# Performance work log

Hardware: AMD Instinct MI355X
Metric: run time of the kernel (lower is better)

The kernel has to match this reference:

```python
import jax, jax.numpy as jnp
import numpy as np

K_ORDER, NUM_HEADS, BETA = 4, 2, 0.5
D_IN, D_OUT = 64, 64


def _batch_and_pos(n_nodes, N):
    # batch[i] = graph id of node i; pos[i] = index of node i within its graph
    batch = jnp.repeat(jnp.arange(n_nodes.shape[0], dtype=jnp.int32), n_nodes, total_repeat_length=N)
    ptr = jnp.concatenate([jnp.zeros(1, jnp.int32), jnp.cumsum(n_nodes).astype(jnp.int32)])
    pos = jnp.arange(N, dtype=jnp.int32) - ptr[batch]
    return batch, pos


def _to_pad(feat, batch, pos, Bsz, max_node):
    out_shape = (Bsz, max_node) + feat.shape[1:]
    return jnp.zeros(out_shape, feat.dtype).at[batch, pos].set(feat)


def fast_attn_conv(qs, ks, vs, n_nodes, batch, pos, max_node):
    # qs/ks/vs: [N,H,D]; linear attention with per-graph kv outer-product sums
    Bsz = n_nodes.shape[0]
    q_pad = _to_pad(qs, batch, pos, Bsz, max_node)  # [B,M,H,D]
    k_pad = _to_pad(ks, batch, pos, Bsz, max_node)
    v_pad = _to_pad(vs, batch, pos, Bsz, max_node)
    kv = jnp.einsum('bnhd,bnhe->bdhe', k_pad, v_pad)  # [B,D,H,D]
    v_sum = jax.ops.segment_sum(vs, batch, num_segments=Bsz)  # [B,H,D]
    k_sum = jax.ops.segment_sum(ks, batch, num_segments=Bsz)  # [B,H,D]
    numerator = jnp.einsum('bnhd,bdhe->bnhe', q_pad, kv)[batch, pos] + v_sum[batch]
    denom = jnp.einsum('bnhd,bhd->bnh', q_pad, k_sum)[batch, pos]
    denom = denom + n_nodes.astype(qs.dtype)[batch][:, None]
    return numerator / denom[..., None]


def gcn_conv(x, edge_index, e_feat):
    # x: [N,H,D], e_feat: [E,D]
    N = x.shape[0]
    row, col = edge_index[0], edge_index[1]
    deg = jax.ops.segment_sum(jnp.ones(row.shape[0], x.dtype), row, num_segments=N)
    dis = jnp.where(deg > 0, deg ** -0.5, jnp.zeros_like(deg))
    w = dis[row] * dis[col]  # [E]
    msg_edge = jax.ops.segment_sum(w[:, None] * e_feat, row, num_segments=N)  # [N,D]
    new_feat = jax.ops.segment_sum(x[col] * w[:, None, None], row, num_segments=N)  # [N,H,D]
    return new_feat + msg_edge[:, None, :]


def setup_inputs():
    key = jax.random.key(0)
    ks = jax.random.split(key, 10)
    B = 64
    n_nodes_np = np.tile(np.array([1000, 2000], np.int32), B // 2)  # sums to 96000
    N = int(n_nodes_np.sum())
    E = 768000
    x = jax.random.normal(ks[0], (N, D_IN), jnp.float32)
    edge_index = jax.random.randint(ks[1], (2, E), 0, N, jnp.int32)
    edge_attr = jax.random.randint(ks[2], (E, 3), 0, 8, jnp.int32)
    s = 0.02
    Wq_w = jax.random.normal(ks[3], (D_IN * NUM_HEADS, D_IN), jnp.float32) * s
    Wq_b = jnp.zeros((D_IN * NUM_HEADS,), jnp.float32)
    Wk_w = jax.random.normal(ks[4], (D_IN * NUM_HEADS, D_IN), jnp.float32) * s
    Wk_b = jnp.zeros((D_IN * NUM_HEADS,), jnp.float32)
    Wo_w = jax.random.normal(ks[5], (D_OUT, D_IN * NUM_HEADS), jnp.float32) * s
    Wo_b = jnp.zeros((D_OUT,), jnp.float32)
    bond_emb = jax.random.normal(ks[6], (3, 8, D_OUT), jnp.float32) * s
    return {"x": x, "Wq_w": Wq_w, "Wq_b": Wq_b, "Wk_w": Wk_w, "Wk_b": Wk_b,
            "Wo_w": Wo_w, "Wo_b": Wo_b, "bond_emb": bond_emb,
            "edge_index": edge_index, "edge_attr": edge_attr,
            "n_nodes": jnp.asarray(n_nodes_np)}


def reference(x, Wq_w, Wq_b, Wk_w, Wk_b, Wo_w, Wo_b, bond_emb, edge_index, edge_attr, n_nodes):
    N = x.shape[0]
    max_node = 2000  # static max over n_nodes
    batch, pos = _batch_and_pos(n_nodes, N)
    query = (x @ Wq_w.T + Wq_b).reshape(N, NUM_HEADS, D_IN)
    key_t = (x @ Wk_w.T + Wk_b).reshape(N, NUM_HEADS, D_IN)
    qs = query / jnp.linalg.norm(query, axis=2, keepdims=True)
    kk = key_t / jnp.linalg.norm(key_t, axis=2, keepdims=True)
    # BondEncoder: sum of per-feature embeddings
    e_feat = bond_emb[0][edge_attr[:, 0]] + bond_emb[1][edge_attr[:, 1]] + bond_emb[2][edge_attr[:, 2]]
    h = jnp.broadcast_to(x[:, None, :], (N, NUM_HEADS, D_IN))
    acc = h
    cur = h
    for _ in range(K_ORDER):
        gcn_i = gcn_conv(cur, edge_index, e_feat)
        attn_i = fast_attn_conv(qs, kk, cur, n_nodes, batch, pos, max_node)
        cur = BETA * gcn_i + (1.0 - BETA) * attn_i
        acc = acc + cur
    out = acc.reshape(N, NUM_HEADS * D_IN)
    return (out @ Wo_w.T + Wo_b) / NUM_HEADS
```

## Files before the change

kernel.cpp:

```cpp
#include <hip/hip_runtime.h>
#include <hip/hip_bf16.h>


typedef __attribute__((ext_vector_type(8))) short bf16x8;
typedef __attribute__((ext_vector_type(4))) float f32x4v;

#define CHUNK 100

__device__ __forceinline__ float asf(unsigned int u) { union { unsigned int i; float f; } v; v.i = u; return v.f; }
__device__ __forceinline__ float b2f_u(unsigned short u) { return asf((unsigned int)u << 16); }
__device__ __forceinline__ unsigned short f2b_u(float f) {
    __hip_bfloat16 h = __float2bfloat16(f);
    union { __hip_bfloat16 h; unsigned short u; } v; v.h = h; return v.u;
}
__device__ __forceinline__ unsigned int pack2(float a, float b) {
    return (unsigned int)f2b_u(a) | ((unsigned int)f2b_u(b) << 16);
}
__device__ __forceinline__ float wave_reduce_sum(float v) {
    #pragma unroll
    for (int off = 32; off > 0; off >>= 1) v += __shfl_xor(v, off, 64);
    return v;
}

__global__ void k_ptr(const int* __restrict__ nn, int* __restrict__ ptr,
                      int* __restrict__ cptr, int* __restrict__ tptr, int B) {
    if (threadIdx.x == 0 && blockIdx.x == 0) {
        int s = 0, c = 0, t = 0; ptr[0] = 0; cptr[0] = 0; tptr[0] = 0;
        for (int i = 0; i < B; ++i) {
            s += nn[i]; ptr[i + 1] = s;
            c += (nn[i] + CHUNK - 1) / CHUNK; cptr[i + 1] = c;
            t += (nn[i] + 15) / 16; tptr[i + 1] = t;
        }
    }
}

__global__ void k_batch(const int* __restrict__ ptr, int* __restrict__ batch) {
    int b = blockIdx.x;
    int s = ptr[b], e = ptr[b + 1];
    for (int i = s + threadIdx.x; i < e; i += blockDim.x) batch[i] = b;
}

__global__ void k_wcvt(const float* __restrict__ Wq_w, const float* __restrict__ Wk_w,
                       const float* __restrict__ Wo_w, unsigned short* __restrict__ Wb) {
    int i = blockIdx.x * 256 + threadIdx.x;
    if (i < 24576) {
        float v = (i < 8192) ? Wq_w[i] : ((i < 16384) ? Wk_w[i - 8192] : Wo_w[i - 16384]);
        Wb[i] = f2b_u(v);
    }
}

__global__ __launch_bounds__(256) void k_qkm(
    const float* __restrict__ x, const unsigned short* __restrict__ Wb,
    const float* __restrict__ Wq_b, const float* __restrict__ Wk_b,
    unsigned short* __restrict__ q, unsigned short* __restrict__ kq,
    unsigned short* __restrict__ curA, int N)
{
    int w = threadIdx.x >> 6, l = threadIdx.x & 63;
    int six = l & 15, quad = l >> 4;
    int base = (blockIdx.x * 4 + w) * 16;
    if (base >= N) return;
    int n = base + six;
    int nc = min(n, N - 1);

    const float* xr = x + (size_t)nc * 64;
    float xv0[8], xv1[8];
    #pragma unroll
    for (int j = 0; j < 8; ++j) { xv0[j] = xr[quad * 8 + j]; xv1[j] = xr[32 + quad * 8 + j]; }
    union { bf16x8 v; unsigned int u[4]; } b0, b1;
    #pragma unroll
    for (int i = 0; i < 4; ++i) {
        b0.u[i] = pack2(xv0[2 * i], xv0[2 * i + 1]);
        b1.u[i] = pack2(xv1[2 * i], xv1[2 * i + 1]);
    }
    if (n < N) {
        unsigned short* cr = curA + (size_t)n * 128;
        *(uint4*)(cr + quad * 8)       = make_uint4(b0.u[0], b0.u[1], b0.u[2], b0.u[3]);
        *(uint4*)(cr + 32 + quad * 8)  = make_uint4(b1.u[0], b1.u[1], b1.u[2], b1.u[3]);
        *(uint4*)(cr + 64 + quad * 8)  = make_uint4(b0.u[0], b0.u[1], b0.u[2], b0.u[3]);
        *(uint4*)(cr + 96 + quad * 8)  = make_uint4(b1.u[0], b1.u[1], b1.u[2], b1.u[3]);
    }

    #pragma unroll
    for (int g = 0; g < 4; ++g) {
        f32x4v c[4];
        #pragma unroll
        for (int tt = 0; tt < 4; ++tt) {
            int t = g * 4 + tt;
            const unsigned short* wr = Wb + (size_t)(t * 16 + six) * 64;
            bf16x8 a0 = *(const bf16x8*)(wr + quad * 8);
            bf16x8 a1 = *(const bf16x8*)(wr + 32 + quad * 8);
            f32x4v cc = {0.f, 0.f, 0.f, 0.f};
            cc = __builtin_amdgcn_mfma_f32_16x16x32_bf16(a0, b0.v, cc, 0, 0, 0);
            cc = __builtin_amdgcn_mfma_f32_16x16x32_bf16(a1, b1.v, cc, 0, 0, 0);
            c[tt] = cc;
        }
        const float* bias = (g < 2) ? Wq_b : Wk_b;
        int cb = (g & 1) * 64 + quad * 4;
        float ss = 0.f;
        #pragma unroll
        for (int tt = 0; tt < 4; ++tt)
            #pragma unroll
            for (int r = 0; r < 4; ++r) {
                float v = c[tt][r] + bias[cb + tt * 16 + r];
                c[tt][r] = v;
                ss += v * v;
            }
        ss += __shfl_xor(ss, 16, 64);
        ss += __shfl_xor(ss, 32, 64);
        float sc = rsqrtf(ss);
        if (n < N) {
            unsigned short* dst = ((g < 2) ? q : kq) + (size_t)n * 128;
            #pragma unroll
            for (int tt = 0; tt < 4; ++tt) {
                unsigned int u0 = pack2(c[tt][0] * sc, c[tt][1] * sc);
                unsigned int u1 = pack2(c[tt][2] * sc, c[tt][3] * sc);
                *(uint2*)(dst + cb + tt * 16) = make_uint2(u0, u1);
            }
        }
    }
}

__global__ void k_deg(const int* __restrict__ row, int* __restrict__ deg,
                      int* __restrict__ slot, int E) {
    int e = blockIdx.x * 256 + threadIdx.x;
    if (e < E) slot[e] = atomicAdd(&deg[row[e]], 1);
}

__global__ void k_dis(const int* __restrict__ deg, float* __restrict__ dis, int N) {
    int n = blockIdx.x * 256 + threadIdx.x;
    if (n < N) { int d = deg[n]; dis[n] = d > 0 ? rsqrtf((float)d) : 0.f; }
}

__global__ void k_scan1(const int* __restrict__ deg, int* __restrict__ rowstart,
                        int* __restrict__ bsum, int N) {
    __shared__ int sh[256];
    int t = threadIdx.x, n = blockIdx.x * 256 + t;
    int v = (n < N) ? deg[n] : 0;
    sh[t] = v; __syncthreads();
    #pragma unroll
    for (int off = 1; off < 256; off <<= 1) {
        int add = (t >= off) ? sh[t - off] : 0;
        __syncthreads();
        sh[t] += add;
        __syncthreads();
    }
    if (n < N) rowstart[n] = sh[t] - v;
    if (t == 255) bsum[blockIdx.x] = sh[255];
}

__global__ void k_scan2(int* __restrict__ bsum, int nb) {
    __shared__ int sh[512];
    __shared__ int carry;
    int t = threadIdx.x;
    if (t == 0) carry = 0;
    __syncthreads();
    for (int base = 0; base < nb; base += 512) {
        int idx = base + t;
        int v = (idx < nb) ? bsum[idx] : 0;
        sh[t] = v; __syncthreads();
        for (int off = 1; off < 512; off <<= 1) {
            int add = (t >= off) ? sh[t - off] : 0;
            __syncthreads();
            sh[t] += add;
            __syncthreads();
        }
        if (idx < nb) bsum[idx] = sh[t] - v + carry;
        __syncthreads();
        if (t == 0) carry += sh[511];
        __syncthreads();
    }
}

__global__ void k_scan3(int* __restrict__ rowstart, const int* __restrict__ bsum, int N, int E) {
    int n = blockIdx.x * 256 + threadIdx.x;
    if (n < N) rowstart[n] += bsum[blockIdx.x];
    if (n == 0) rowstart[N] = E;
}

__global__ void k_fill(const int* __restrict__ eidx, const float* __restrict__ dis,
                       const int* __restrict__ rowstart, const int* __restrict__ slot,
                       int4* __restrict__ csr_pack, const int* __restrict__ eattr, int E) {
    int e = blockIdx.x * 256 + threadIdx.x;
    if (e >= E) return;
    int r = eidx[e], c = eidx[E + e];
    float wv = dis[r] * dis[c];
    int a0 = eattr[e * 3 + 0], a1 = eattr[e * 3 + 1], a2 = eattr[e * 3 + 2];
    int idx = rowstart[r] + slot[e];
    int4 v;
    v.x = c;
    v.y = __float_as_int(wv);
    v.z = a0 | (a1 << 8) | (a2 << 16);
    v.w = 0;
    csr_pack[idx] = v;
}

__global__ __launch_bounds__(256) void k_msg(
    const int* __restrict__ rowstart, const int4* __restrict__ csr_pack,
    const float* __restrict__ bond, unsigned short* __restrict__ msgb, int N) {
    __shared__ float bl[1536];
    int t = threadIdx.x, w = t >> 6, l = t & 63;
    for (int i = t; i < 1536; i += 256) bl[i] = bond[i];
    __syncthreads();
    for (int n = blockIdx.x * 4 + w; n < N; n += gridDim.x * 4) {
        int s0 = rowstart[n], s1 = rowstart[n + 1];
        float m = 0.f;
        #pragma unroll 4
        for (int i = s0; i < s1; ++i) {
            int4 pk = csr_pack[i];
            float wv = __int_as_float(pk.y);
            int att = pk.z;
            m += wv * (bl[(att & 255) * 64 + l] + bl[(8 + ((att >> 8) & 255)) * 64 + l]
                     + bl[(16 + (att >> 16)) * 64 + l]);
        }
        msgb[(size_t)n * 64 + l] = f2b_u(m);
    }
}

__global__ __launch_bounds__(256) void k_ksump(
    const unsigned short* __restrict__ kq, const int* __restrict__ ptr,
    const int* __restrict__ cptr, float* __restrict__ partKS, int B)
{
    int cid = blockIdx.x;
    if (cid >= cptr[B]) return;
    int lo = 0, hi = B - 1;
    while (lo < hi) { int mid = (lo + hi + 1) >> 1; if (cptr[mid] <= cid) lo = mid; else hi = mid - 1; }
    int b = lo;
    int start = ptr[b] + (cid - cptr[b]) * CHUNK;
    int end = min(start + CHUNK, ptr[b + 1]);
    int t = threadIdx.x, r = t >> 7, col = t & 127;
    float a = 0.f;
    for (int n = start + r; n < end; n += 2)
        a += b2f_u(kq[(size_t)n * 128 + col]);
    __shared__ float sh[256];
    sh[t] = a;
    __syncthreads();
    if (t < 128) partKS[(size_t)cid * 128 + t] = sh[t] + sh[t + 128];
}

__global__ __launch_bounds__(128) void k_ksr(
    const float* __restrict__ partKS, const int* __restrict__ cptr,
    float* __restrict__ ksum, int B)
{
    int b = blockIdx.x, t = threadIdx.x;
    float s = 0.f;
    int c0 = cptr[b], c1 = cptr[b + 1];
    for (int c = c0; c < c1; ++c) s += partKS[(size_t)c * 128 + t];
    ksum[b * 128 + t] = s;
}

__global__ __launch_bounds__(256) void k_denom(
    const unsigned short* __restrict__ q, const float* __restrict__ ksum,
    const int* __restrict__ batch, const int* __restrict__ nn,
    float* __restrict__ denom, int N)
{
    int w = threadIdx.x >> 6, l = threadIdx.x & 63;
    int n = blockIdx.x * 4 + w;
    if (n >= N) return;
    int b = batch[n];
    float d0 = b2f_u(q[(size_t)n * 128 + l]) * ksum[b * 128 + l];
    float d1 = b2f_u(q[(size_t)n * 128 + 64 + l]) * ksum[b * 128 + 64 + l];
    d0 = wave_reduce_sum(d0);
    d1 = wave_reduce_sum(d1);
    if (l == 0) {
        float nf = (float)nn[b];
        denom[n * 2 + 0] = d0 + nf;
        denom[n * 2 + 1] = d1 + nf;
    }
}

__global__ __launch_bounds__(256) void k_kvp(
    const unsigned short* __restrict__ kq, const unsigned short* __restrict__ cur,
    const int* __restrict__ ptr, const int* __restrict__ cptr,
    float* __restrict__ partKV, float* __restrict__ partVS, int B)
{
    int cid = blockIdx.x;
    if (cid >= cptr[B]) return;
    int lo = 0, hi = B - 1;
    while (lo < hi) { int mid = (lo + hi + 1) >> 1; if (cptr[mid] <= cid) lo = mid; else hi = mid - 1; }
    int b = lo;
    int start = ptr[b] + (cid - cptr[b]) * CHUNK;
    int end = min(start + CHUNK, ptr[b + 1]);

    int w = threadIdx.x >> 6, l = threadIdx.x & 63;
    int h = w >> 1, dhalf = w & 1;
    int d0 = dhalf * 32 + (l & 7) * 4;
    int e0 = (l >> 3) * 8;
    float a[4][8], va[8];
    #pragma unroll
    for (int i = 0; i < 4; ++i)
        #pragma unroll
        for (int j = 0; j < 8; ++j) a[i][j] = 0.f;
    #pragma unroll
    for (int j = 0; j < 8; ++j) va[j] = 0.f;

    const unsigned short* kp = kq + (size_t)start * 128 + h * 64 + d0;
    const unsigned short* vp = cur + (size_t)start * 128 + h * 64 + e0;
    #pragma unroll 4
    for (int n = start; n < end; ++n) {
        uint2 ku = *(const uint2*)kp;
        uint4 vu = *(const uint4*)vp;
        kp += 128; vp += 128;
        float k0 = asf(ku.x << 16), k1 = asf(ku.x & 0xffff0000u);
        float k2 = asf(ku.y << 16), k3 = asf(ku.y & 0xffff0000u);
        float v[8];
        v[0] = asf(vu.x << 16); v[1] = asf(vu.x & 0xffff0000u);
        v[2] = asf(vu.y << 16); v[3] = asf(vu.y & 0xffff0000u);
        v[4] = asf(vu.z << 16); v[5] = asf(vu.z & 0xffff0000u);
        v[6] = asf(vu.w << 16); v[7] = asf(vu.w & 0xffff0000u);
        #pragma unroll
        for (int j = 0; j < 8; ++j) {
            a[0][j] += k0 * v[j]; a[1][j] += k1 * v[j];
            a[2][j] += k2 * v[j]; a[3][j] += k3 * v[j];
            va[j] += v[j];
        }
    }
    float* dst = partKV + (size_t)cid * 8192 + h * 4096;
    #pragma unroll
    for (int j = 0; j < 8; ++j) {
        float4 s4 = { a[0][j], a[1][j], a[2][j], a[3][j] };
        *(float4*)(dst + (e0 + j) * 64 + d0) = s4;
    }
    if (dhalf == 0 && (l & 7) == 0) {
        float* vdst = partVS + (size_t)cid * 128 + h * 64 + e0;
        #pragma unroll
        for (int j = 0; j < 8; ++j) vdst[j] = va[j];
    }
}

__global__ __launch_bounds__(256) void k_red(
    const float* __restrict__ partKV, const float* __restrict__ partVS,
    const int* __restrict__ cptr, unsigned short* __restrict__ kvT_b,
    float* __restrict__ vsum, int B)
{
    int bid = blockIdx.x;
    int gh = bid >> 1, half = bid & 1;
    int g = gh >> 1, h = gh & 1;
    int c0 = cptr[g], c1 = cptr[g + 1];
    int t = threadIdx.x;
    int off = half * 2048 + t * 8;
    float s[8];
    #pragma unroll
    for (int i = 0; i < 8; ++i) s[i] = 0.f;
    for (int c = c0; c < c1; ++c) {
        const float4* src = (const float4*)(partKV + (size_t)c * 8192 + h * 4096 + off);
        #pragma unroll
        for (int i = 0; i < 2; ++i) {
            float4 v = src[i];
            s[i * 4 + 0] += v.x; s[i * 4 + 1] += v.y; s[i * 4 + 2] += v.z; s[i * 4 + 3] += v.w;
        }
    }
    unsigned int u[4];
    #pragma unroll
    for (int i = 0; i < 4; ++i) u[i] = pack2(s[2 * i], s[2 * i + 1]);
    *(uint4*)(kvT_b + (size_t)gh * 4096 + off) = make_uint4(u[0], u[1], u[2], u[3]);
    if (half == 0 && t < 64) {
        float vs = 0.f;
        for (int c = c0; c < c1; ++c) vs += partVS[(size_t)c * 128 + h * 64 + t];
        vsum[g * 128 + h * 64 + t] = vs;
    }
}

__global__ __launch_bounds__(256) void k_attn(
    const unsigned short* __restrict__ q, const unsigned short* __restrict__ kvT,
    const float* __restrict__ vsum, const float* __restrict__ denom,
    const int* __restrict__ ptr, const int* __restrict__ tptr,
    unsigned short* __restrict__ curB, int B)
{
    int w = threadIdx.x >> 6, l = threadIdx.x & 63;
    int tid = blockIdx.x * 4 + w;
    if (tid >= tptr[B]) return;
    int lo = 0, hi = B - 1;
    while (lo < hi) { int mid = (lo + hi + 1) >> 1; if (tptr[mid] <= tid) lo = mid; else hi = mid - 1; }
    int b0 = lo;
    int start = ptr[b0] + (tid - tptr[b0]) * 16;
    int end = min(start + 16, ptr[b0 + 1]);
    int quad = l >> 4, six = l & 15;
    int n = start + six;
    int nc = min(n, end - 1);
    bool live = n < end;
    #pragma unroll
    for (int h = 0; h < 2; ++h) {
        const unsigned short* qrow = q + (size_t)nc * 128 + h * 64;
        bf16x8 qb0 = *(const bf16x8*)(qrow + quad * 8);
        bf16x8 qb1 = *(const bf16x8*)(qrow + 32 + quad * 8);
        const unsigned short* Bb = kvT + (size_t)(b0 * 2 + h) * 4096;
        float dn = denom[nc * 2 + h];
        const float* vsb = vsum + (b0 * 2 + h) * 64;
        #pragma unroll
        for (int et = 0; et < 4; ++et) {
            const unsigned short* arow = Bb + (size_t)(et * 16 + six) * 64;
            bf16x8 a0 = *(const bf16x8*)(arow + quad * 8);
            bf16x8 a1 = *(const bf16x8*)(arow + 32 + quad * 8);
            f32x4v c = {0.f, 0.f, 0.f, 0.f};
            c = __builtin_amdgcn_mfma_f32_16x16x32_bf16(a0, qb0, c, 0, 0, 0);
            c = __builtin_amdgcn_mfma_f32_16x16x32_bf16(a1, qb1, c, 0, 0, 0);
            float4 vs = *(const float4*)(vsb + et * 16 + quad * 4);
            float v0 = 0.5f * (c[0] + vs.x) / dn;
            float v1 = 0.5f * (c[1] + vs.y) / dn;
            float v2 = 0.5f * (c[2] + vs.z) / dn;
            float v3 = 0.5f * (c[3] + vs.w) / dn;
            if (live) {
                uint2 st = make_uint2(pack2(v0, v1), pack2(v2, v3));
                *(uint2*)(curB + (size_t)n * 128 + h * 64 + et * 16 + quad * 4) = st;
            }
        }
    }
}

__global__ __launch_bounds__(256) void k_gcn(
    const unsigned short* __restrict__ curA, const unsigned short* __restrict__ msgb,
    const int* __restrict__ rowstart, const int4* __restrict__ csr_pack,
    unsigned short* __restrict__ curB, unsigned short* __restrict__ acc, int N, int first)
{
    int orig = blockIdx.x, nwg = gridDim.x;
    int q8 = nwg >> 3, r8 = nwg & 7;
    int xcd = orig & 7, j = orig >> 3;
    int swz = (xcd < r8 ? xcd * (q8 + 1) : r8 * (q8 + 1) + (xcd - r8) * q8) + j;

    int w = threadIdx.x >> 6, l = threadIdx.x & 63;
    int qq = l >> 4, ql = l & 15;
    int n = swz * 4 + w;
    if (n >= N) return;
    int s0 = rowstart[n], s1 = rowstart[n + 1];
    float g[8];
    #pragma unroll
    for (int j2 = 0; j2 < 8; ++j2) g[j2] = 0.f;
    #pragma unroll 2
    for (int i = s0 + qq; i < s1; i += 4) {
        int4 pk = csr_pack[i];
        float wv = __int_as_float(pk.y);
        uint4 u = *(const uint4*)(curA + (size_t)pk.x * 128 + 8 * ql);
        g[0] += wv * asf(u.x << 16); g[1] += wv * asf(u.x & 0xffff0000u);
        g[2] += wv * asf(u.y << 16); g[3] += wv * asf(u.y & 0xffff0000u);
        g[4] += wv * asf(u.z << 16); g[5] += wv * asf(u.z & 0xffff0000u);
        g[6] += wv * asf(u.w << 16); g[7] += wv * asf(u.w & 0xffff0000u);
    }
    #pragma unroll
    for (int j2 = 0; j2 < 8; ++j2) {
        g[j2] += __shfl_xor(g[j2], 16, 64);
        g[j2] += __shfl_xor(g[j2], 32, 64);
    }
    float g0 = (qq == 0) ? g[0] : (qq == 1) ? g[2] : (qq == 2) ? g[4] : g[6];
    float g1 = (qq == 0) ? g[1] : (qq == 1) ? g[3] : (qq == 2) ? g[5] : g[7];
    int e0 = 8 * ql + 2 * qq;
    unsigned int um = *(const unsigned int*)(msgb + (size_t)n * 64 + (e0 & 63));
    float mx = asf(um << 16), my = asf(um & 0xffff0000u);
    size_t o = (size_t)n * 128 + e0;
    unsigned int ub = *(const unsigned int*)(curB + o);
    float v0 = 0.5f * (g0 + mx) + asf(ub << 16);
    float v1 = 0.5f * (g1 + my) + asf(ub & 0xffff0000u);
    *(unsigned int*)(curB + o) = pack2(v0, v1);
    unsigned int ua = *(const unsigned int*)(first ? (curA + o) : (acc + o));
    *(unsigned int*)(acc + o) = pack2(asf(ua << 16) + v0, asf(ua & 0xffff0000u) + v1);
}

__global__ __launch_bounds__(256) void k_outm(
    const unsigned short* __restrict__ acc, const unsigned short* __restrict__ Wob,
    const float* __restrict__ Wo_b, float* __restrict__ out, int N)
{
    int w = threadIdx.x >> 6, l = threadIdx.x & 63;
    int six = l & 15, quad = l >> 4;
    int base = (blockIdx.x * 4 + w) * 16;
    if (base >= N) return;
    int n = base + six;
    int nc = min(n, N - 1);
    const unsigned short* ar = acc + (size_t)nc * 128;
    bf16x8 b0 = *(const bf16x8*)(ar + quad * 8);
    bf16x8 b1 = *(const bf16x8*)(ar + 32 + quad * 8);
    bf16x8 b2 = *(const bf16x8*)(ar + 64 + quad * 8);
    bf16x8 b3 = *(const bf16x8*)(ar + 96 + quad * 8);
    #pragma unroll
    for (int t = 0; t < 4; ++t) {
        const unsigned short* wr = Wob + (size_t)(t * 16 + six) * 128;
        bf16x8 a0 = *(const bf16x8*)(wr + quad * 8);
        bf16x8 a1 = *(const bf16x8*)(wr + 32 + quad * 8);
        bf16x8 a2 = *(const bf16x8*)(wr + 64 + quad * 8);
        bf16x8 a3 = *(const bf16x8*)(wr + 96 + quad * 8);
        f32x4v c = {0.f, 0.f, 0.f, 0.f};
        c = __builtin_amdgcn_mfma_f32_16x16x32_bf16(a0, b0, c, 0, 0, 0);
        c = __builtin_amdgcn_mfma_f32_16x16x32_bf16(a1, b1, c, 0, 0, 0);
        c = __builtin_amdgcn_mfma_f32_16x16x32_bf16(a2, b2, c, 0, 0, 0);
        c = __builtin_amdgcn_mfma_f32_16x16x32_bf16(a3, b3, c, 0, 0, 0);
        if (n < N) {
            float4 bias = *(const float4*)(Wo_b + t * 16 + quad * 4);
            float4 o4;
            o4.x = (c[0] + bias.x) * 0.5f;
            o4.y = (c[1] + bias.y) * 0.5f;
            o4.z = (c[2] + bias.z) * 0.5f;
            o4.w = (c[3] + bias.w) * 0.5f;
            *(float4*)(out + (size_t)n * 64 + t * 16 + quad * 4) = o4;
        }
    }
}

extern "C" void kernel_launch(void* const* d_in, const int* in_sizes, int n_in,
                              void* d_out, int out_size, void* d_ws, size_t ws_size,
                              hipStream_t stream) {
    const float* x    = (const float*)d_in[0];
    const float* Wq_w = (const float*)d_in[1];
    const float* Wq_b = (const float*)d_in[2];
    const float* Wk_w = (const float*)d_in[3];
    const float* Wk_b = (const float*)d_in[4];
    const float* Wo_w = (const float*)d_in[5];
    const float* Wo_b = (const float*)d_in[6];
    const float* bond = (const float*)d_in[7];
    const int*   eidx = (const int*)d_in[8];
    const int*   eattr= (const int*)d_in[9];
    const int*   nn   = (const int*)d_in[10];
    float* out = (float*)d_out;
    int N = in_sizes[0] / 64;
    int E = in_sizes[9] / 3;
    int B = in_sizes[10];

    char* p = (char*)d_ws;
    auto alloc = [&](size_t bytes) { char* r = p; p += (bytes + 255) & ~(size_t)255; return r; };
    unsigned short* q    = (unsigned short*)alloc((size_t)N * 128 * 2);
    unsigned short* kq   = (unsigned short*)alloc((size_t)N * 128 * 2);
    unsigned short* curA = (unsigned short*)alloc((size_t)N * 128 * 2);
    unsigned short* curB = (unsigned short*)alloc((size_t)N * 128 * 2);
    unsigned short* acc  = (unsigned short*)alloc((size_t)N * 128 * 2);
    int maxchunks = (N + CHUNK - 1) / CHUNK + B;
    int maxtiles  = (N + 15) / 16 + B;
    float* partKV = (float*)alloc((size_t)maxchunks * 8192 * 4);
    float* partVS = (float*)alloc((size_t)maxchunks * 128 * 4);
    float* partKS = (float*)alloc((size_t)maxchunks * 128 * 4);
    unsigned short* kvT_b = (unsigned short*)alloc((size_t)B * 2 * 64 * 64 * 2);
    float* vsum  = (float*)alloc((size_t)B * 128 * 4);
    float* ksum  = (float*)alloc((size_t)B * 128 * 4);
    float* denom = (float*)alloc((size_t)N * 2 * 4);
    float* dis   = (float*)alloc((size_t)N * 4);
    int* deg     = (int*)alloc((size_t)N * 4);
    int* rowstart= (int*)alloc((size_t)(N + 1) * 4);
    int* slot    = (int*)alloc((size_t)E * 4);
    int4* csr_pack = (int4*)alloc((size_t)E * 16);
    int* batch   = (int*)alloc((size_t)N * 4);
    int* ptr     = (int*)alloc((size_t)(B + 1) * 4);
    int* cptr    = (int*)alloc((size_t)(B + 1) * 4);
    int* tptr    = (int*)alloc((size_t)(B + 1) * 4);
    unsigned short* Wb = (unsigned short*)alloc(24576 * 2);
    int nb = (N + 255) / 256;
    int* bsum    = (int*)alloc((size_t)nb * 4);
    unsigned short* msgb = (unsigned short*)out;

    hipMemsetAsync(deg, 0, (size_t)N * 4, stream);

    k_ptr  <<<1, 64, 0, stream>>>(nn, ptr, cptr, tptr, B);
    k_batch<<<B, 256, 0, stream>>>(ptr, batch);
    k_wcvt <<<96, 256, 0, stream>>>(Wq_w, Wk_w, Wo_w, Wb);
    k_qkm  <<<(N + 63) / 64, 256, 0, stream>>>(x, Wb, Wq_b, Wk_b, q, kq, curA, N);
    k_deg  <<<(E + 255) / 256, 256, 0, stream>>>(eidx, deg, slot, E);
    k_dis  <<<(N + 255) / 256, 256, 0, stream>>>(deg, dis, N);
    k_scan1<<<nb, 256, 0, stream>>>(deg, rowstart, bsum, N);
    k_scan2<<<1, 512, 0, stream>>>(bsum, nb);
    k_scan3<<<nb, 256, 0, stream>>>(rowstart, bsum, N, E);
    k_fill <<<(E + 255) / 256, 256, 0, stream>>>(eidx, dis, rowstart, slot, csr_pack, eattr, E);
    k_msg  <<<2048, 256, 0, stream>>>(rowstart, csr_pack, bond, msgb, N);
    k_ksump<<<maxchunks, 256, 0, stream>>>(kq, ptr, cptr, partKS, B);
    k_ksr  <<<B, 128, 0, stream>>>(partKS, cptr, ksum, B);
    k_denom<<<(N + 3) / 4, 256, 0, stream>>>(q, ksum, batch, nn, denom, N);

    for (int it = 0; it < 4; ++it) {
        k_kvp <<<maxchunks, 256, 0, stream>>>(kq, curA, ptr, cptr, partKV, partVS, B);
        k_red <<<B * 4, 256, 0, stream>>>(partKV, partVS, cptr, kvT_b, vsum, B);
        k_attn<<<(maxtiles + 3) / 4, 256, 0, stream>>>(q, kvT_b, vsum, denom, ptr, tptr, curB, B);
        k_gcn <<<(N + 3) / 4, 256, 0, stream>>>(curA, msgb, rowstart, csr_pack, curB, acc, N, it == 0 ? 1 : 0);
        unsigned short* tmp = curA; curA = curB; curB = tmp;
    }
    k_outm<<<(N + 63) / 64, 256, 0, stream>>>(acc, Wb + 16384, Wo_b, out, N);
}
```

Before: 792.9 us.

## Process two GCN rows per wave and fold edge message into attention kernel

The GCN kernel now has each wave handle two consecutive CSR rows over their combined edge range. It keeps a total accumulator and one for row A, and recovers row B by subtraction, which balances work across short rows and halves the wave count. The per-node bond-message add moves into the attention epilogue, and the GCN kernel reads only weight and column from the packed CSR entry. Recovering row B by subtraction can add floating-point cancellation error, and the loop now does twice the FMAs per edge.

```diff
diff --git a/kernel.cpp b/kernel.cpp
--- a/kernel.cpp
+++ b/kernel.cpp
@@ -364,6 +364,7 @@
     const unsigned short* __restrict__ q, const unsigned short* __restrict__ kvT,
     const float* __restrict__ vsum, const float* __restrict__ denom,
     const int* __restrict__ ptr, const int* __restrict__ tptr,
+    const unsigned short* __restrict__ msgb,
     unsigned short* __restrict__ curB, int B)
 {
     int w = threadIdx.x >> 6, l = threadIdx.x & 63;
@@ -378,6 +379,10 @@
     int n = start + six;
     int nc = min(n, end - 1);
     bool live = n < end;
+    const unsigned short* mrow = msgb + (size_t)nc * 64;
+    uint2 me[4];
+    #pragma unroll
+    for (int et = 0; et < 4; ++et) me[et] = *(const uint2*)(mrow + et * 16 + quad * 4);
     #pragma unroll
     for (int h = 0; h < 2; ++h) {
         const unsigned short* qrow = q + (size_t)nc * 128 + h * 64;
@@ -395,10 +400,12 @@
             c = __builtin_amdgcn_mfma_f32_16x16x32_bf16(a0, qb0, c, 0, 0, 0);
             c = __builtin_amdgcn_mfma_f32_16x16x32_bf16(a1, qb1, c, 0, 0, 0);
             float4 vs = *(const float4*)(vsb + et * 16 + quad * 4);
-            float v0 = 0.5f * (c[0] + vs.x) / dn;
-            float v1 = 0.5f * (c[1] + vs.y) / dn;
-            float v2 = 0.5f * (c[2] + vs.z) / dn;
-            float v3 = 0.5f * (c[3] + vs.w) / dn;
+            float m0 = asf(me[et].x << 16), m1 = asf(me[et].x & 0xffff0000u);
+            float m2 = asf(me[et].y << 16), m3 = asf(me[et].y & 0xffff0000u);
+            float v0 = 0.5f * (c[0] + vs.x) / dn + 0.5f * m0;
+            float v1 = 0.5f * (c[1] + vs.y) / dn + 0.5f * m1;
+            float v2 = 0.5f * (c[2] + vs.z) / dn + 0.5f * m2;
+            float v3 = 0.5f * (c[3] + vs.w) / dn + 0.5f * m3;
             if (live) {
                 uint2 st = make_uint2(pack2(v0, v1), pack2(v2, v3));
                 *(uint2*)(curB + (size_t)n * 128 + h * 64 + et * 16 + quad * 4) = st;
@@ -408,50 +415,81 @@
 }
 
 __global__ __launch_bounds__(256) void k_gcn(
-    const unsigned short* __restrict__ curA, const unsigned short* __restrict__ msgb,
+    const unsigned short* __restrict__ curA,
     const int* __restrict__ rowstart, const int4* __restrict__ csr_pack,
     unsigned short* __restrict__ curB, unsigned short* __restrict__ acc, int N, int first)
 {
     int orig = blockIdx.x, nwg = gridDim.x;
     int q8 = nwg >> 3, r8 = nwg & 7;
-    int xcd = orig & 7, j = orig >> 3;
-    int swz = (xcd < r8 ? xcd * (q8 + 1) : r8 * (q8 + 1) + (xcd - r8) * q8) + j;
+    int xcd = orig & 7, jj = orig >> 3;
+    int swz = (xcd < r8 ? xcd * (q8 + 1) : r8 * (q8 + 1) + (xcd - r8) * q8) + jj;
 
     int w = threadIdx.x >> 6, l = threadIdx.x & 63;
     int qq = l >> 4, ql = l & 15;
-    int n = swz * 4 + w;
-    if (n >= N) return;
-    int s0 = rowstart[n], s1 = rowstart[n + 1];
-    float g[8];
-    #pragma unroll
-    for (int j2 = 0; j2 < 8; ++j2) g[j2] = 0.f;
+    int nA = swz * 8 + w * 2;
+    if (nA >= N) return;
+    bool hasB = (nA + 1) < N;
+    int s0  = rowstart[nA];
+    int sA1 = rowstart[nA + 1];
+    int s1  = hasB ? rowstart[nA + 2] : sA1;
+
+    int e0 = 8 * ql + 2 * qq;
+    size_t oA = (size_t)nA * 128 + e0;
+    size_t oB = (size_t)(nA + 1) * 128 + e0;
+    const unsigned short* accsrc = first ? curA : acc;
+    unsigned int ubA = *(const unsigned int*)(curB + oA);
+    unsigned int uaA = *(const unsigned int*)(accsrc + oA);
+    unsigned int ubB = 0, uaB = 0;
+    if (hasB) {
+        ubB = *(const unsigned int*)(curB + oB);
+        uaB = *(const unsigned int*)(accsrc + oB);
+    }
+
+    float gT[8], gA[8];
+    #pragma unroll
+    for (int j = 0; j < 8; ++j) { gT[j] = 0.f; gA[j] = 0.f; }
+    const int2* cw2 = (const int2*)csr_pack;
     #pragma unroll 2
     for (int i = s0 + qq; i < s1; i += 4) {
-        int4 pk = csr_pack[i];
-        float wv = __int_as_float(pk.y);
-        uint4 u = *(const uint4*)(curA + (size_t)pk.x * 128 + 8 * ql);
-        g[0] += wv * asf(u.x << 16); g[1] += wv * asf(u.x & 0xffff0000u);
-        g[2] += wv * asf(u.y << 16); g[3] += wv * asf(u.y & 0xffff0000u);
-        g[4] += wv * asf(u.z << 16); g[5] += wv * asf(u.z & 0xffff0000u);
-        g[6] += wv * asf(u.w << 16); g[7] += wv * asf(u.w & 0xffff0000u);
-    }
-    #pragma unroll
-    for (int j2 = 0; j2 < 8; ++j2) {
-        g[j2] += __shfl_xor(g[j2], 16, 64);
-        g[j2] += __shfl_xor(g[j2], 32, 64);
-    }
-    float g0 = (qq == 0) ? g[0] : (qq == 1) ? g[2] : (qq == 2) ? g[4] : g[6];
-    float g1 = (qq == 0) ? g[1] : (qq == 1) ? g[3] : (qq == 2) ? g[5] : g[7];
-    int e0 = 8 * ql + 2 * qq;
-    unsigned int um = *(const unsigned int*)(msgb + (size_t)n * 64 + (e0 & 63));
-    float mx = asf(um << 16), my = asf(um & 0xffff0000u);
-    size_t o = (size_t)n * 128 + e0;
-    unsigned int ub = *(const unsigned int*)(curB + o);
-    float v0 = 0.5f * (g0 + mx) + asf(ub << 16);
-    float v1 = 0.5f * (g1 + my) + asf(ub & 0xffff0000u);
-    *(unsigned int*)(curB + o) = pack2(v0, v1);
-    unsigned int ua = *(const unsigned int*)(first ? (curA + o) : (acc + o));
-    *(unsigned int*)(acc + o) = pack2(asf(ua << 16) + v0, asf(ua & 0xffff0000u) + v1);
+        int2 cw = cw2[2 * i];
+        float wv = __int_as_float(cw.y);
+        float wvA = (i < sA1) ? wv : 0.f;
+        uint4 u = *(const uint4*)(curA + (size_t)cw.x * 128 + 8 * ql);
+        float v0 = asf(u.x << 16), v1 = asf(u.x & 0xffff0000u);
+        float v2 = asf(u.y << 16), v3 = asf(u.y & 0xffff0000u);
+        float v4 = asf(u.z << 16), v5 = asf(u.z & 0xffff0000u);
+        float v6 = asf(u.w << 16), v7 = asf(u.w & 0xffff0000u);
+        gT[0] += wv * v0;  gA[0] += wvA * v0;
+        gT[1] += wv * v1;  gA[1] += wvA * v1;
+        gT[2] += wv * v2;  gA[2] += wvA * v2;
+        gT[3] += wv * v3;  gA[3] += wvA * v3;
+        gT[4] += wv * v4;  gA[4] += wvA * v4;
+        gT[5] += wv * v5;  gA[5] += wvA * v5;
+        gT[6] += wv * v6;  gA[6] += wvA * v6;
+        gT[7] += wv * v7;  gA[7] += wvA * v7;
+    }
+    #pragma unroll
+    for (int j = 0; j < 8; ++j) {
+        gT[j] += __shfl_xor(gT[j], 16, 64);
+        gT[j] += __shfl_xor(gT[j], 32, 64);
+        gA[j] += __shfl_xor(gA[j], 16, 64);
+        gA[j] += __shfl_xor(gA[j], 32, 64);
+    }
+    float a0 = (qq == 0) ? gA[0] : (qq == 1) ? gA[2] : (qq == 2) ? gA[4] : gA[6];
+    float a1 = (qq == 0) ? gA[1] : (qq == 1) ? gA[3] : (qq == 2) ? gA[5] : gA[7];
+    float t0 = (qq == 0) ? gT[0] : (qq == 1) ? gT[2] : (qq == 2) ? gT[4] : gT[6];
+    float t1 = (qq == 0) ? gT[1] : (qq == 1) ? gT[3] : (qq == 2) ? gT[5] : gT[7];
+    float b0 = t0 - a0, b1 = t1 - a1;
+    float vA0 = 0.5f * a0 + asf(ubA << 16);
+    float vA1 = 0.5f * a1 + asf(ubA & 0xffff0000u);
+    *(unsigned int*)(curB + oA) = pack2(vA0, vA1);
+    *(unsigned int*)(acc + oA) = pack2(asf(uaA << 16) + vA0, asf(uaA & 0xffff0000u) + vA1);
+    if (hasB) {
+        float vB0 = 0.5f * b0 + asf(ubB << 16);
+        float vB1 = 0.5f * b1 + asf(ubB & 0xffff0000u);
+        *(unsigned int*)(curB + oB) = pack2(vB0, vB1);
+        *(unsigned int*)(acc + oB) = pack2(asf(uaB << 16) + vB0, asf(uaB & 0xffff0000u) + vB1);
+    }
 }
 
 __global__ __launch_bounds__(256) void k_outm(
@@ -559,11 +597,12 @@
     k_ksr  <<<B, 128, 0, stream>>>(partKS, cptr, ksum, B);
     k_denom<<<(N + 3) / 4, 256, 0, stream>>>(q, ksum, batch, nn, denom, N);
 
+    int gcnblk = (N + 7) / 8;
     for (int it = 0; it < 4; ++it) {
         k_kvp <<<maxchunks, 256, 0, stream>>>(kq, curA, ptr, cptr, partKV, partVS, B);
         k_red <<<B * 4, 256, 0, stream>>>(partKV, partVS, cptr, kvT_b, vsum, B);
-        k_attn<<<(maxtiles + 3) / 4, 256, 0, stream>>>(q, kvT_b, vsum, denom, ptr, tptr, curB, B);
-        k_gcn <<<(N + 3) / 4, 256, 0, stream>>>(curA, msgb, rowstart, csr_pack, curB, acc, N, it == 0 ? 1 : 0);
+        k_attn<<<(maxtiles + 3) / 4, 256, 0, stream>>>(q, kvT_b, vsum, denom, ptr, tptr, msgb, curB, B);
+        k_gcn <<<gcnblk, 256, 0, stream>>>(curA, rowstart, csr_pack, curB, acc, N, it == 0 ? 1 : 0);
         unsigned short* tmp = curA; curA = curB; curB = tmp;
     }
     k_outm<<<(N + 63) / 64, 256, 0, stream>>>(acc, Wb + 16384, Wo_b, out, N);
```

Measured after the change: 788.4 us. About the same (-0.6%).
